# Kernel tuning notes

Measured on AMD Instinct MI355X. Metric: run time of the kernel, lower is better.

The kernel has to match this reference:

```python
import jax, jax.numpy as jnp
import numpy as np

B, T, IN, H, G, O, D = 64, 256, 256, 1024, 256, 64, 4
GO = G + O  # graph_size + out_channels = 320


def _lstm_cell(x, h, c, Wih, Whh, bih, bhh):
    # torch.nn.LSTMCell gate order: i, f, g, o
    g = x @ Wih.T + h @ Whh.T + (bih + bhh)
    i, f, gg, o = jnp.split(g, 4, axis=-1)
    c_new = jax.nn.sigmoid(f) * c + jax.nn.sigmoid(i) * jnp.tanh(gg)
    h_new = jax.nn.sigmoid(o) * jnp.tanh(c_new)
    return h_new, c_new


def _mlp(x, W1, b1, W2, b2, W3, b3):
    # make_mlp with linear_depth=3: Linear->SiLU->Linear->SiLU->Linear
    x = jax.nn.silu(x @ W1.T + b1)
    x = jax.nn.silu(x @ W2.T + b2)
    return x @ W3.T + b3


def setup_inputs() -> dict:
    key = jax.random.key(0)
    ks = iter(jax.random.split(key, 64))
    def p(shape, s=0.05):
        return jax.random.normal(next(ks), shape, jnp.float32) * s
    inp = {}
    inp["z"] = jax.random.normal(next(ks), (B, IN), jnp.float32)
    inp["m_true"] = jax.random.normal(next(ks), (B, T, GO), jnp.float32)
    for pre, od in (("eh", H), ("ec", H), ("ex", O)):
        inp[pre + "_W1"] = p((H, IN)); inp[pre + "_b1"] = p((H,))
        inp[pre + "_W2"] = p((H, H));  inp[pre + "_b2"] = p((H,))
        inp[pre + "_W3"] = p((od, H)); inp[pre + "_b3"] = p((od,))
    inp["in_Wih"] = p((4 * H, GO)); inp["in_Whh"] = p((4 * H, H))
    inp["in_bih"] = p((4 * H,));    inp["in_bhh"] = p((4 * H,))
    inp["rnns_Wih"] = p((D, 4 * H, H)); inp["rnns_Whh"] = p((D, 4 * H, H))
    inp["rnns_bih"] = p((D, 4 * H));    inp["rnns_bhh"] = p((D, 4 * H))
    inp["hA_W"] = p((D, H, H)); inp["hA_b"] = p((D, H))
    inp["cA_W"] = p((D, H, H)); inp["cA_b"] = p((D, H))
    inp["lastH_W"] = p((GO, H)); inp["lastH_b"] = p((GO,))
    inp["lastC_W"] = p((GO, H)); inp["lastC_b"] = p((GO,))
    inp["out_Wih"] = p((4 * GO, H)); inp["out_Whh"] = p((4 * GO, GO))
    inp["out_bih"] = p((4 * GO,));   inp["out_bhh"] = p((4 * GO,))
    return inp


def reference(z, m_true,
              eh_W1, eh_b1, eh_W2, eh_b2, eh_W3, eh_b3,
              ec_W1, ec_b1, ec_W2, ec_b2, ec_W3, ec_b3,
              ex_W1, ex_b1, ex_W2, ex_b2, ex_W3, ex_b3,
              in_Wih, in_Whh, in_bih, in_bhh,
              rnns_Wih, rnns_Whh, rnns_bih, rnns_bhh,
              hA_W, hA_b, cA_W, cA_b,
              lastH_W, lastH_b, lastC_W, lastC_b,
              out_Wih, out_Whh, out_bih, out_bhh):
    h0 = _mlp(z, eh_W1, eh_b1, eh_W2, eh_b2, eh_W3, eh_b3)
    c0 = _mlp(z, ec_W1, ec_b1, ec_W2, ec_b2, ec_W3, ec_b3)
    x_last = _mlp(z, ex_W1, ex_b1, ex_W2, ex_b2, ex_W3, ex_b3)
    m_hat0 = jnp.concatenate(
        [jnp.zeros((z.shape[0], G), z.dtype), x_last], axis=-1)  # [B, GO]
    # flip time, use first T-1 steps; time-major for scan: [T-1, B, GO]
    mt = jnp.flip(m_true, axis=1)[:, :-1, :].transpose(1, 0, 2)

    def step(carry, m_t):
        h0_, c0_ = carry
        h2, c2 = _lstm_cell(m_t, h0_, c0_, in_Wih, in_Whh, in_bih, in_bhh)
        c1 = c2
        for i in range(D):  # recurrent_depth inner chain (fixed, structural)
            h1 = h2 @ hA_W[i].T + hA_b[i]
            c1 = c2 @ cA_W[i].T + cA_b[i]
            h2, c2 = _lstm_cell(h2, h1, c1,
                                rnns_Wih[i], rnns_Whh[i],
                                rnns_bih[i], rnns_bhh[i])
        # note: original reuses c1 (last adapter output) for last_c_adapter
        hh = h2 @ lastH_W.T + lastH_b
        cc = c1 @ lastC_W.T + lastC_b
        ho, _ = _lstm_cell(h2, hh, cc, out_Wih, out_Whh, out_bih, out_bhh)
        return (h2, c2), ho

    _, outs = jax.lax.scan(step, (h0, c0), mt)  # outs: [T-1, B, GO]
    m_hat = jnp.concatenate([m_hat0[:, None, :], outs.transpose(1, 0, 2)],
                            axis=1)  # [B, T, GO]
    return m_hat
```

## Files before the change

### kernel.cpp

```cpp
#include <hip/hip_runtime.h>


typedef unsigned int u32;
typedef unsigned long long u64;
typedef unsigned short u16;
typedef __attribute__((ext_vector_type(8))) __bf16 bf16x8;
typedef __attribute__((ext_vector_type(4))) float f32x4;

#define DEVI __device__ __forceinline__

union FRAG { bf16x8 v; u16 s[8]; u64 q[2]; };
union P4 { u64 q; u16 s[4]; };
union F4 { u64 q[2]; float f[4]; };

DEVI u16 f2bf(float x){ u32 u = __float_as_uint(x); return (u16)((u + 0x7fffu + ((u>>16)&1u)) >> 16); }
DEVI float sigm(float x){ return 1.0f/(1.0f + __expf(-x)); }
DEVI float tanh_(float x){ return 2.0f/(1.0f + __expf(-2.0f*x)) - 1.0f; }
DEVI void ast(void* p, u64 v){ __hip_atomic_store((u64*)p, v, __ATOMIC_RELAXED, __HIP_MEMORY_SCOPE_AGENT); }

DEVI void ld16sc(FRAG& d, const void* p){
  asm volatile("global_load_dwordx4 %0, %1, off sc0 sc1" : "=v"(d.v) : "v"(p));
}
DEVI void ld16(FRAG& d, const void* p){
  asm volatile("global_load_dwordx4 %0, %1, off" : "=v"(d.v) : "v"(p));
}
DEVI void ldf4(f32x4& d, const void* p){
  asm volatile("global_load_dwordx4 %0, %1, off" : "=v"(d) : "v"(p));
}

#define MFMA16(a,b,c) __builtin_amdgcn_mfma_f32_16x16x32_bf16(a, b, c, 0, 0, 0)

#define NWG 168

#define SCHEDB() __builtin_amdgcn_sched_barrier(0)
#define WAITV(n) do{ SCHEDB(); \
  asm volatile("s_waitcnt vmcnt(" #n ")" ::: "memory"); \
  SCHEDB(); }while(0)

__global__ __launch_bounds__(256, 1) void k_scan(
    const float* __restrict__ m_true,
    const u16* __restrict__ Wcell, const u16* __restrict__ Win_h,
    const u16* __restrict__ Win_x, const u16* __restrict__ Wout,
    const u16* __restrict__ WccA,
    const float* __restrict__ b_in, const float* __restrict__ b_cell,
    const float* __restrict__ cAb, const float* __restrict__ b_out,
    const float* __restrict__ b_cc,
    u16* hS, u16* cS, float* cF, float* outp, u32* bar)
{
  const int wg = blockIdx.x;
  const int tid = threadIdx.x;
  const int wave = tid >> 6, lane = tid & 63;

  int pipe, lw;
  if (wg < 160){ pipe = (wg >> 3) & 1; lw = ((wg >> 4) << 3) | (wg & 7); }
  else         { pipe = (wg - 160) >> 2; lw = 80 + ((wg - 160) & 3); }

  const int bl = lane & 15, kg = lane >> 4;
  const int pair = wave >> 1;
  const int bt = (pipe << 1) + (wave & 1);
  const int b  = (bt << 4) + bl;
  const int swz = (bl & 7) << 4;
  const int foff = ((bl << 2) + kg) << 4;
  const int woff = (bt << 15) + ((lw >> 1) << 10) + (bl << 6) + ((lw & 1) << 5) + (kg << 3);
  u32* flagp = bar + (pipe*128 + lw)*32;
  const u32* fbase = bar + pipe*128*32;
  const int i2 = (lane < 20) ? 64 + lane : lane;
  __shared__ __align__(16) u16 ldsW[81920];

  f32x4 cprev = {0,0,0,0};
  f32x4 ccreg = {0,0,0,0};

  auto stage1 = [&](const u16* src, u16* lb, int segs){
    const u16* g = src + (lane << 3);
    u16* l = lb;
    for (int s = 0; s < segs; ++s){
      __builtin_amdgcn_global_load_lds(
          (const __attribute__((address_space(1))) void*)g,
          (__attribute__((address_space(3))) void*)l, 16, 0, 0);
      g += 512; l += 512;
    }
    SCHEDB();
  };
  auto afL = [&](const u16* lb, int row, int kb) -> bf16x8 {
    return *(const bf16x8*)((const char*)lb + row*512 + (kb ^ swz));
  };

  auto gsync = [&](u32 ep, const u16* pfsrc, int cstride, int spw, const u16* xsrc){
    SCHEDB();
    __syncthreads();
    if (tid == 0)
      __hip_atomic_store(flagp, ep, __ATOMIC_RELAXED, __HIP_MEMORY_SCOPE_AGENT);
    SCHEDB();
    if (pfsrc) stage1(pfsrc + (size_t)wave*cstride, ldsW + wave*cstride, spw);
    if (xsrc)  stage1(xsrc + wave*4096, ldsW + 65536 + wave*4096, 8);
    SCHEDB();
    if (wave == 0){
      for(;;){
        u32 a = __hip_atomic_load(fbase + lane*32, __ATOMIC_RELAXED, __HIP_MEMORY_SCOPE_AGENT);
        u32 c2 = __hip_atomic_load(fbase + i2*32, __ATOMIC_RELAXED, __HIP_MEMORY_SCOPE_AGENT);
        if (__all(a >= ep && c2 >= ep)) break;
        __builtin_amdgcn_s_sleep(1);
      }
    }
    __syncthreads();
    SCHEDB();
  };

  auto phase_incell = [&](int t, const u16* hIn, u16* hOut, u16* cOut){
    f32x4 A0={0,0,0,0}, A1={0,0,0,0}, A2={0,0,0,0}, A3={0,0,0,0};
    const char* hf = (const char*)hIn + (bt << 15) + foff;
    const int ksb = pair << 4;
    int jl = (kg << 2), jj = (lw << 4) + jl;
    FRAG sh[2][8], pa[8];
    f32x4 bg0, bg1, bg2, bg3;
    #pragma unroll
    for (int ks = 0; ks < 8; ++ks) ld16sc(sh[0][ks], hf + (ksb + ks)*1024);
    #pragma unroll
    for (int ks = 0; ks < 8; ++ks) ld16sc(sh[1][ks], hf + (ksb + 8 + ks)*1024);
    {
      const char* p2 = (const char*)(Win_x + (size_t)lw*20480 + 16384);
      #pragma unroll
      for (int k2 = 0; k2 < 2; ++k2)
        #pragma unroll
        for (int rb = 0; rb < 4; ++rb)
          ld16(pa[k2*4+rb], p2 + (rb*16 + bl)*128 + (((k2<<6)+(kg<<4)) ^ swz));
    }
    ldf4(bg0, b_in +        jj);
    ldf4(bg1, b_in + 1024 + jj);
    ldf4(bg2, b_in + 2048 + jj);
    ldf4(bg3, b_in + 3072 + jj);
    WAITV(20);
    const u16* lbA = ldsW + (pair*2)*16384;
    #pragma unroll
    for (int ks = 0; ks < 8; ++ks){
      int kb = (ks << 6) + (kg << 4);
      FRAG a;
      a.v = afL(lbA, bl, kb);      A0 = MFMA16(a.v, sh[0][ks].v, A0);
      a.v = afL(lbA, 16 + bl, kb); A1 = MFMA16(a.v, sh[0][ks].v, A1);
      a.v = afL(lbA, 32 + bl, kb); A2 = MFMA16(a.v, sh[0][ks].v, A2);
      a.v = afL(lbA, 48 + bl, kb); A3 = MFMA16(a.v, sh[0][ks].v, A3);
    }
    WAITV(12);
    const u16* lbB = ldsW + (pair*2+1)*16384;
    #pragma unroll
    for (int ks = 0; ks < 8; ++ks){
      int kb = (ks << 6) + (kg << 4);
      FRAG a;
      a.v = afL(lbB, bl, kb);      A0 = MFMA16(a.v, sh[1][ks].v, A0);
      a.v = afL(lbB, 16 + bl, kb); A1 = MFMA16(a.v, sh[1][ks].v, A1);
      a.v = afL(lbB, 32 + bl, kb); A2 = MFMA16(a.v, sh[1][ks].v, A2);
      a.v = afL(lbB, 48 + bl, kb); A3 = MFMA16(a.v, sh[1][ks].v, A3);
    }
    WAITV(4);
    if (wave >= 2){
      FRAG xf[10];
      const float* xr = m_true + (size_t)b*81920 + (size_t)(255 - t)*320;
      #pragma unroll
      for (int ks = 0; ks < 10; ++ks){
        int k = (ks << 5) + (kg << 3);
        f32x4 x0 = *(const f32x4*)(xr + k);
        f32x4 x1 = *(const f32x4*)(xr + k + 4);
        xf[ks].s[0]=f2bf(x0[0]); xf[ks].s[1]=f2bf(x0[1]); xf[ks].s[2]=f2bf(x0[2]); xf[ks].s[3]=f2bf(x0[3]);
        xf[ks].s[4]=f2bf(x1[0]); xf[ks].s[5]=f2bf(x1[1]); xf[ks].s[6]=f2bf(x1[2]); xf[ks].s[7]=f2bf(x1[3]);
      }
      const u16* lb4 = ldsW + 65536;
      #pragma unroll
      for (int ks = 0; ks < 8; ++ks){
        int kb = (ks << 6) + (kg << 4);
        FRAG a;
        a.v = afL(lb4, bl, kb);      A0 = MFMA16(a.v, xf[ks].v, A0);
        a.v = afL(lb4, 16 + bl, kb); A1 = MFMA16(a.v, xf[ks].v, A1);
        a.v = afL(lb4, 32 + bl, kb); A2 = MFMA16(a.v, xf[ks].v, A2);
        a.v = afL(lb4, 48 + bl, kb); A3 = MFMA16(a.v, xf[ks].v, A3);
      }
      #pragma unroll
      for (int k2 = 0; k2 < 2; ++k2){
        A0 = MFMA16(pa[k2*4+0].v, xf[8+k2].v, A0);
        A1 = MFMA16(pa[k2*4+1].v, xf[8+k2].v, A1);
        A2 = MFMA16(pa[k2*4+2].v, xf[8+k2].v, A2);
        A3 = MFMA16(pa[k2*4+3].v, xf[8+k2].v, A3);
      }
    }
    __syncthreads();
    float* red = (float*)ldsW;
    if (wave >= 2){
      float* r = red + ((wave&1)*64 + lane)*20;
      *(f32x4*)(r+0) = A0; *(f32x4*)(r+4) = A1;
      *(f32x4*)(r+8) = A2; *(f32x4*)(r+12) = A3;
    }
    __syncthreads();
    if (wave < 2){
      const float* r = red + ((wave&1)*64 + lane)*20;
      A0 += *(const f32x4*)(r+0); A1 += *(const f32x4*)(r+4);
      A2 += *(const f32x4*)(r+8); A3 += *(const f32x4*)(r+12);
      P4 hw, cw;
      #pragma unroll
      for (int rr = 0; rr < 4; ++rr){
        float gi = A0[rr] + bg0[rr];
        float gf = A1[rr] + bg1[rr];
        float gg = A2[rr] + bg2[rr];
        float go = A3[rr] + bg3[rr];
        float cn = sigm(gf)*cprev[rr] + sigm(gi)*tanh_(gg);
        hw.s[rr] = f2bf(sigm(go)*tanh_(cn));
        cw.s[rr] = f2bf(cn);
      }
      ast((char*)hOut + woff, hw.q);
      ast((char*)cOut + woff, cw.q);
    }
  };

  auto phase_cell = [&](int i, const u16* hIn, const u16* cIn, u16* hOut, u16* cOut, bool last){
    f32x4 A0={0,0,0,0}, A1={0,0,0,0}, A2={0,0,0,0}, A3={0,0,0,0}, A4={0,0,0,0};
    const char* hf  = (const char*)hIn + (bt << 15) + foff;
    const char* cfr = (const char*)cIn + (bt << 15) + foff;
    const int ksb = pair << 4;
    int jl = (kg << 2), jj = (lw << 4) + jl;
    FRAG sh[2][8], sc[2][8];
    f32x4 bg0, bg1, bg2, bg3, bca;
    #pragma unroll
    for (int ks = 0; ks < 8; ++ks) ld16sc(sh[0][ks], hf  + (ksb + ks)*1024);
    #pragma unroll
    for (int ks = 0; ks < 8; ++ks) ld16sc(sc[0][ks], cfr + (ksb + ks)*1024);
    #pragma unroll
    for (int ks = 0; ks < 8; ++ks) ld16sc(sh[1][ks], hf  + (ksb + 8 + ks)*1024);
    #pragma unroll
    for (int ks = 0; ks < 8; ++ks) ld16sc(sc[1][ks], cfr + (ksb + 8 + ks)*1024);
    ldf4(bg0, b_cell + i*4096 +        jj);
    ldf4(bg1, b_cell + i*4096 + 1024 + jj);
    ldf4(bg2, b_cell + i*4096 + 2048 + jj);
    ldf4(bg3, b_cell + i*4096 + 3072 + jj);
    ldf4(bca, cAb + i*1024 + jj);
    WAITV(21);
    const u16* lbA = ldsW + (pair*2)*20480;
    #pragma unroll
    for (int ks = 0; ks < 8; ++ks){
      int kb = (ks << 6) + (kg << 4);
      FRAG a;
      a.v = afL(lbA, bl, kb);      A0 = MFMA16(a.v, sh[0][ks].v, A0);
      a.v = afL(lbA, 16 + bl, kb); A1 = MFMA16(a.v, sh[0][ks].v, A1);
      a.v = afL(lbA, 32 + bl, kb); A2 = MFMA16(a.v, sh[0][ks].v, A2);
      a.v = afL(lbA, 48 + bl, kb); A3 = MFMA16(a.v, sh[0][ks].v, A3);
      a.v = afL(lbA, 64 + bl, kb); A4 = MFMA16(a.v, sc[0][ks].v, A4);
    }
    WAITV(5);
    const u16* lbB = ldsW + (pair*2+1)*20480;
    #pragma unroll
    for (int ks = 0; ks < 8; ++ks){
      int kb = (ks << 6) + (kg << 4);
      FRAG a;
      a.v = afL(lbB, bl, kb);      A0 = MFMA16(a.v, sh[1][ks].v, A0);
      a.v = afL(lbB, 16 + bl, kb); A1 = MFMA16(a.v, sh[1][ks].v, A1);
      a.v = afL(lbB, 32 + bl, kb); A2 = MFMA16(a.v, sh[1][ks].v, A2);
      a.v = afL(lbB, 48 + bl, kb); A3 = MFMA16(a.v, sh[1][ks].v, A3);
      a.v = afL(lbB, 64 + bl, kb); A4 = MFMA16(a.v, sc[1][ks].v, A4);
    }
    __syncthreads();
    float* red = (float*)ldsW;
    if (wave >= 2){
      float* r = red + ((wave&1)*64 + lane)*20;
      *(f32x4*)(r+0) = A0; *(f32x4*)(r+4) = A1;
      *(f32x4*)(r+8) = A2; *(f32x4*)(r+12) = A3; *(f32x4*)(r+16) = A4;
    }
    __syncthreads();
    if (wave < 2){
      const float* r = red + ((wave&1)*64 + lane)*20;
      A0 += *(const f32x4*)(r+0); A1 += *(const f32x4*)(r+4);
      A2 += *(const f32x4*)(r+8); A3 += *(const f32x4*)(r+12);
      A4 += *(const f32x4*)(r+16);
      P4 hw, cw; F4 cf4;
      #pragma unroll
      for (int rr = 0; rr < 4; ++rr){
        float gi = A0[rr] + bg0[rr];
        float gf = A1[rr] + bg1[rr];
        float gg = A2[rr] + bg2[rr];
        float go = A3[rr] + bg3[rr];
        float c1 = A4[rr] + bca[rr];
        float cn = sigm(gf)*c1 + sigm(gi)*tanh_(gg);
        hw.s[rr] = f2bf(sigm(go)*tanh_(cn));
        cw.s[rr] = f2bf(cn);
        cf4.f[rr] = cn;
      }
      ast((char*)hOut + woff, hw.q);
      ast((char*)cOut + woff, cw.q);
      if (last){ cprev[0]=cf4.f[0]; cprev[1]=cf4.f[1]; cprev[2]=cf4.f[2]; cprev[3]=cf4.f[3]; }
    }
  };

  auto phase_ccA = [&](const u16* cIn){
    f32x4 A = {0,0,0,0};
    const char* cfr = (const char*)cIn + (bt << 15) + foff;
    const int ksb = pair << 4;
    int jl = (kg << 2), jjo = ((lw - 64) << 4) + jl;
    FRAG sc[2][8];
    f32x4 bcc;
    #pragma unroll
    for (int ks = 0; ks < 8; ++ks) ld16sc(sc[0][ks], cfr + (ksb + ks)*1024);
    #pragma unroll
    for (int ks = 0; ks < 8; ++ks) ld16sc(sc[1][ks], cfr + (ksb + 8 + ks)*1024);
    ldf4(bcc, b_cc + jjo);
    WAITV(9);
    const u16* lbA = ldsW + (pair*2)*4096;
    #pragma unroll
    for (int ks = 0; ks < 8; ++ks){
      int kb = (ks << 6) + (kg << 4);
      FRAG a; a.v = afL(lbA, bl, kb);
      A = MFMA16(a.v, sc[0][ks].v, A);
    }
    WAITV(1);
    const u16* lbB = ldsW + (pair*2+1)*4096;
    #pragma unroll
    for (int ks = 0; ks < 8; ++ks){
      int kb = (ks << 6) + (kg << 4);
      FRAG a; a.v = afL(lbB, bl, kb);
      A = MFMA16(a.v, sc[1][ks].v, A);
    }
    __syncthreads();
    float* red = (float*)ldsW;
    if (wave >= 2) *(f32x4*)(red + ((wave&1)*64 + lane)*20) = A;
    __syncthreads();
    if (wave < 2){
      A += *(const f32x4*)(red + ((wave&1)*64 + lane)*20);
      #pragma unroll
      for (int rr = 0; rr < 4; ++rr) ccreg[rr] = A[rr] + bcc[rr];
    }
  };

  auto phase_out = [&](int t, const u16* hIn){
    f32x4 A0={0,0,0,0}, A1={0,0,0,0}, A2={0,0,0,0}, A3={0,0,0,0};
    const char* hf = (const char*)hIn + (bt << 15) + foff;
    const int ksb = pair << 4;
    int jl = (kg << 2), jjo = ((lw - 64) << 4) + jl;
    FRAG sh[2][8];
    f32x4 bg0, bg1, bg2, bg3;
    #pragma unroll
    for (int ks = 0; ks < 8; ++ks) ld16sc(sh[0][ks], hf + (ksb + ks)*1024);
    #pragma unroll
    for (int ks = 0; ks < 8; ++ks) ld16sc(sh[1][ks], hf + (ksb + 8 + ks)*1024);
    ldf4(bg0, b_out +       jjo);
    ldf4(bg1, b_out + 320 + jjo);
    ldf4(bg2, b_out + 640 + jjo);
    ldf4(bg3, b_out + 960 + jjo);
    WAITV(12);
    const u16* lbA = ldsW + (pair*2)*16384;
    #pragma unroll
    for (int ks = 0; ks < 8; ++ks){
      int kb = (ks << 6) + (kg << 4);
      FRAG a;
      a.v = afL(lbA, bl, kb);      A0 = MFMA16(a.v, sh[0][ks].v, A0);
      a.v = afL(lbA, 16 + bl, kb); A1 = MFMA16(a.v, sh[0][ks].v, A1);
      a.v = afL(lbA, 32 + bl, kb); A2 = MFMA16(a.v, sh[0][ks].v, A2);
      a.v = afL(lbA, 48 + bl, kb); A3 = MFMA16(a.v, sh[0][ks].v, A3);
    }
    WAITV(4);
    const u16* lbB = ldsW + (pair*2+1)*16384;
    #pragma unroll
    for (int ks = 0; ks < 8; ++ks){
      int kb = (ks << 6) + (kg << 4);
      FRAG a;
      a.v = afL(lbB, bl, kb);      A0 = MFMA16(a.v, sh[1][ks].v, A0);
      a.v = afL(lbB, 16 + bl, kb); A1 = MFMA16(a.v, sh[1][ks].v, A1);
      a.v = afL(lbB, 32 + bl, kb); A2 = MFMA16(a.v, sh[1][ks].v, A2);
      a.v = afL(lbB, 48 + bl, kb); A3 = MFMA16(a.v, sh[1][ks].v, A3);
    }
    __syncthreads();
    float* red = (float*)ldsW;
    if (wave >= 2){
      float* r = red + ((wave&1)*64 + lane)*20;
      *(f32x4*)(r+0) = A0; *(f32x4*)(r+4) = A1;
      *(f32x4*)(r+8) = A2; *(f32x4*)(r+12) = A3;
    }
    __syncthreads();
    if (wave < 2){
      const float* r = red + ((wave&1)*64 + lane)*20;
      A0 += *(const f32x4*)(r+0); A1 += *(const f32x4*)(r+4);
      A2 += *(const f32x4*)(r+8); A3 += *(const f32x4*)(r+12);
      f32x4 ho;
      #pragma unroll
      for (int rr = 0; rr < 4; ++rr){
        float gi = A0[rr] + bg0[rr];
        float gf = A1[rr] + bg1[rr];
        float gg = A2[rr] + bg2[rr];
        float go = A3[rr] + bg3[rr];
        float cn = sigm(gf)*ccreg[rr] + sigm(gi)*tanh_(gg);
        ho[rr] = sigm(go)*tanh_(cn);
      }
      *(f32x4*)(outp + (size_t)b*81920 + (size_t)(t+1)*320 + jjo) = ho;
    }
  };

  if (lw < 64){
    if (wave < 2){
      int jj = (lw << 4) + (kg << 2);
      cprev = *(const f32x4*)(cF + (size_t)b*1024 + jj);
    }
    stage1(Win_h + ((size_t)lw << 16) + wave*16384, ldsW + wave*16384, 32);
    stage1(Win_x + (size_t)lw*20480 + wave*4096, ldsW + 65536 + wave*4096, 8);
  }
  __syncthreads();
  SCHEDB();

  u16* hB0 = hS;        u16* hB1 = hS + 65536;
  u16* cB0 = cS;        u16* cB1 = cS + 65536;

  u32 ep = 1;
  if (lw < 64) phase_incell(0, hB1, hB0, cB0);
  gsync(ep++, (lw < 64) ? Wcell + (size_t)lw*81920 : nullptr, 20480, 40, nullptr);
  int p = 1;
  #pragma unroll 1
  for (int t = 0; t < 255; ++t){
    #pragma unroll 1
    for (int i = 0; i < 4; ++i){
      u16* hIn = (p & 1) ? hB0 : hB1;  u16* cIn = (p & 1) ? cB0 : cB1;
      u16* hOut = (p & 1) ? hB1 : hB0; u16* cOut = (p & 1) ? cB1 : cB0;
      if (lw < 64)      phase_cell(i, hIn, cIn, hOut, cOut, i == 3);
      else if (i == 3)  phase_ccA(cIn);
      const u16* pf = nullptr; const u16* xs = nullptr; int cstride = 0, spw = 0;
      if (lw < 64){
        if (i < 3){ pf = Wcell + (size_t)((i+1)*64 + lw)*81920; cstride = 20480; spw = 40; }
        else      { pf = Win_h + ((size_t)lw << 16); cstride = 16384; spw = 32;
                    xs = Win_x + (size_t)lw*20480; }
      } else {
        if (i == 2){ pf = WccA + ((size_t)(lw-64) << 14); cstride = 4096; spw = 8; }
        else if (i == 3){ pf = Wout + ((size_t)(lw-64) << 16); cstride = 16384; spw = 32; }
      }
      gsync(ep++, pf, cstride, spw, xs);
      ++p;
    }
    u16* hIn = (p & 1) ? hB0 : hB1;
    u16* hOut = (p & 1) ? hB1 : hB0; u16* cOut = (p & 1) ? cB1 : cB0;
    if (lw >= 64)       phase_out(t, hIn);
    else if (t < 254)   phase_incell(t + 1, hIn, hOut, cOut);
    gsync(ep++, (lw < 64 && t < 254) ? Wcell + (size_t)lw*81920 : nullptr, 20480, 40, nullptr);
    ++p;
  }
}


__global__ __launch_bounds__(256) void k_dense(const float* __restrict__ X, int xmode,
    const float* __restrict__ W, const float* __restrict__ bias,
    int OD, int ID, int act, int omode, float* outF, u16* outB)
{
  int o = blockIdx.x*4 + (threadIdx.x >> 6);
  if (o >= OD) return;
  int lane = threadIdx.x & 63;
  const float* wr = W + (size_t)o*ID;
  float acc = 0.f;
  if (xmode == 0){ for (int k = 0; k < ID; ++k) acc = fmaf(wr[k], X[(size_t)lane*ID + k], acc); }
  else           { for (int k = 0; k < ID; ++k) acc = fmaf(wr[k], X[(size_t)k*64 + lane], acc); }
  acc += bias[o];
  if (act) acc = acc * sigm(acc);
  if (omode == 0)      outF[(size_t)o*64 + lane] = acc;
  else if (omode == 1){
    int bt = lane >> 4, blx = lane & 15;
    outB[(size_t)bt*16384 + (size_t)(o>>5)*512 + blx*32 + ((o&31)>>3)*8 + (o&7)] = f2bf(acc);
  }
  else if (omode == 2) outF[(size_t)lane*1024 + o] = acc;
  else                 outF[(size_t)lane*81920 + 256 + o] = acc;
}

__global__ void k_zero0(float* out){ out[(size_t)blockIdx.x*81920 + threadIdx.x] = 0.f; }

__global__ __launch_bounds__(256) void k_tr(const float* __restrict__ in, u16* __restrict__ out, int M, int N){
  __shared__ u16 t[64][65];
  int m0 = blockIdx.x << 6, n0 = blockIdx.y << 6;
  int c = threadIdx.x & 63, rq = threadIdx.x >> 6;
  for (int rr = 0; rr < 16; ++rr){
    int r = (rq << 4) + rr;
    t[r][c] = f2bf(in[(size_t)(m0 + r)*N + n0 + c]);
  }
  __syncthreads();
  for (int rr = 0; rr < 16; ++rr){
    int r = (rq << 4) + rr;
    out[(size_t)(n0 + r)*M + m0 + c] = t[c][r];
  }
}

__global__ __launch_bounds__(256) void k_fuse(const float* __restrict__ Whh, const float* __restrict__ Wih,
    const u16* __restrict__ BT, int KM, int mode, u16* __restrict__ dst)
{
  int bx = blockIdx.x, by = blockIdx.y, bz = blockIdx.z;
  int lane = threadIdx.x & 63, wv = threadIdx.x >> 6;
  int bl = lane & 15, kg = lane >> 4;
  int jbase = (mode == 0) ? bz*1024 : ((mode == 1) ? bz*320 : 0);
  int jrow = jbase + bx*16 + bl;
  int k2c = by*64 + wv*16 + bl;
  f32x4 acc = {0,0,0,0};
  for (int m0 = 0; m0 < KM; m0 += 32){
    f32x4 wa0 = *(const f32x4*)(Whh + (size_t)jrow*KM + m0 + (kg << 3));
    f32x4 wa1 = *(const f32x4*)(Whh + (size_t)jrow*KM + m0 + (kg << 3) + 4);
    FRAG a;
    a.s[0]=f2bf(wa0[0]); a.s[1]=f2bf(wa0[1]); a.s[2]=f2bf(wa0[2]); a.s[3]=f2bf(wa0[3]);
    a.s[4]=f2bf(wa1[0]); a.s[5]=f2bf(wa1[1]); a.s[6]=f2bf(wa1[2]); a.s[7]=f2bf(wa1[3]);
    FRAG bb; bb.v = *(const bf16x8*)(BT + (size_t)k2c*KM + m0 + (kg << 3));
    acc = MFMA16(a.v, bb.v, acc);
  }
  #pragma unroll
  for (int r = 0; r < 4; ++r){
    int jl = (kg << 2) + r;
    int jg = jbase + bx*16 + jl;
    float v = acc[r];
    if (mode < 2) v += Wih[(size_t)jg*1024 + k2c];
    int re = (mode == 2) ? jl : (bz*16 + jl);
    int c = k2c >> 8, kl = k2c & 255;
    size_t pos;
    if (mode == 0)      pos = (size_t)bx*81920 + c*20480 + re*256 + (kl ^ ((re&7)<<3));
    else if (mode == 1) pos = (size_t)bx*65536 + c*16384 + re*256 + (kl ^ ((re&7)<<3));
    else                pos = (size_t)bx*16384 + c*4096  + re*256 + (kl ^ ((re&7)<<3));
    dst[pos] = f2bf(v);
  }
}

__global__ void k_pack_winh(const float* __restrict__ src, u16* __restrict__ dst){
  int id = blockIdx.x*256 + threadIdx.x;
  int j = id >> 10, k = id & 1023;
  int g = j >> 10, jj = j & 1023;
  int w = jj >> 4, r = (g << 4) + (jj & 15);
  int c = k >> 8, kl = k & 255;
  dst[(size_t)w*65536 + c*16384 + r*256 + (kl ^ ((r&7)<<3))] = f2bf(src[id]);
}

__global__ void k_pack_winx(const float* __restrict__ src, u16* __restrict__ dst){
  int j = blockIdx.x, k = threadIdx.x;
  int g = j >> 10, jj = j & 1023;
  int w = jj >> 4, r = (g << 4) + (jj & 15);
  float v = src[(size_t)j*320 + k];
  size_t pos;
  if (k < 256) pos = (size_t)w*20480 + r*256 + (k ^ ((r&7)<<3));
  else         pos = (size_t)w*20480 + 16384 + r*64 + ((k - 256) ^ ((r&7)<<3));
  dst[pos] = f2bf(v);
}

__global__ void k_pack_ca(const float* __restrict__ src, u16* __restrict__ dst){
  int id = blockIdx.x*256 + threadIdx.x;
  int jj = id >> 10, k = id & 1023;
  int w = jj >> 4, r = 64 + (jj & 15);
  int c = k >> 8, kl = k & 255;
  dst[(size_t)w*81920 + c*20480 + r*256 + (kl ^ ((r&7)<<3))] = f2bf(src[id]);
}

__global__ __launch_bounds__(256) void k_bias(const float* __restrict__ A, const float* __restrict__ x,
    const float* __restrict__ a1, const float* __restrict__ a2, float* __restrict__ o, int NJ, int K)
{
  int j = blockIdx.x*4 + (threadIdx.x >> 6);
  if (j >= NJ) return;
  int lane = threadIdx.x & 63;
  float acc = 0.f;
  if (A) for (int k = lane; k < K; k += 64) acc += A[(size_t)j*K + k]*x[k];
  for (int off = 32; off; off >>= 1) acc += __shfl_down(acc, off);
  if (lane == 0) o[j] = acc + (a1 ? a1[j] : 0.f) + (a2 ? a2[j] : 0.f);
}

extern "C" void kernel_launch(void* const* d_in, const int* in_sizes, int n_in,
                              void* d_out, int out_size, void* d_ws, size_t ws_size,
                              hipStream_t stream)
{
  (void)in_sizes; (void)n_in; (void)out_size;
  const float* z      = (const float*)d_in[0];
  const float* m_true = (const float*)d_in[1];
  const float* eh_W1=(const float*)d_in[2],  *eh_b1=(const float*)d_in[3];
  const float* eh_W2=(const float*)d_in[4],  *eh_b2=(const float*)d_in[5];
  const float* eh_W3=(const float*)d_in[6],  *eh_b3=(const float*)d_in[7];
  const float* ec_W1=(const float*)d_in[8],  *ec_b1=(const float*)d_in[9];
  const float* ec_W2=(const float*)d_in[10], *ec_b2=(const float*)d_in[11];
  const float* ec_W3=(const float*)d_in[12], *ec_b3=(const float*)d_in[13];
  const float* ex_W1=(const float*)d_in[14], *ex_b1=(const float*)d_in[15];
  const float* ex_W2=(const float*)d_in[16], *ex_b2=(const float*)d_in[17];
  const float* ex_W3=(const float*)d_in[18], *ex_b3=(const float*)d_in[19];
  const float* in_Wih=(const float*)d_in[20], *in_Whh=(const float*)d_in[21];
  const float* in_bih=(const float*)d_in[22], *in_bhh=(const float*)d_in[23];
  const float* r_Wih=(const float*)d_in[24],  *r_Whh=(const float*)d_in[25];
  const float* r_bih=(const float*)d_in[26],  *r_bhh=(const float*)d_in[27];
  const float* hA_W=(const float*)d_in[28],   *hA_b=(const float*)d_in[29];
  const float* cA_W=(const float*)d_in[30],   *cA_b=(const float*)d_in[31];
  const float* lastH_W=(const float*)d_in[32], *lastH_b=(const float*)d_in[33];
  const float* lastC_W=(const float*)d_in[34], *lastC_b=(const float*)d_in[35];
  const float* out_Wih=(const float*)d_in[36], *out_Whh=(const float*)d_in[37];
  const float* out_bih=(const float*)d_in[38], *out_bhh=(const float*)d_in[39];
  float* out = (float*)d_out;

  char* wsb = (char*)d_ws;
  size_t off = 0;
  auto alloc = [&](size_t bytes)->char*{
    char* p = wsb + off; off = (off + bytes + 255) & ~(size_t)255; return p;
  };
  u32* bar    = (u32*)alloc(256*32*4);
  u16* hS     = (u16*)alloc(2*64*1024*2);
  u16* cS     = (u16*)alloc(2*64*1024*2);
  float* cF   = (float*)alloc(64*1024*4);
  float* b_in = (float*)alloc(4096*4);
  float* b_cell=(float*)alloc(4*4096*4);
  float* b_out= (float*)alloc(1280*4);
  float* b_cc = (float*)alloc(320*4);
  float* t1   = (float*)alloc(1024*64*4);
  float* t2   = (float*)alloc(1024*64*4);
  u16* Tbuf   = (u16*)alloc((size_t)1024*1024*2);
  u16* Win_h  = (u16*)alloc((size_t)64*65536*2);
  u16* Win_x  = (u16*)alloc((size_t)64*20480*2);
  u16* Wcell  = (u16*)alloc((size_t)4*64*81920*2);
  u16* Wout   = (u16*)alloc((size_t)20*65536*2);
  u16* WccA   = (u16*)alloc((size_t)20*16384*2);
  if (off > ws_size) return;

  hipMemsetAsync(bar, 0, 256*32*4, stream);

  k_dense<<<256,256,0,stream>>>(z, 0, eh_W1, eh_b1, 1024, 256, 1, 0, t1, nullptr);
  k_dense<<<256,256,0,stream>>>(t1,1, eh_W2, eh_b2, 1024,1024, 1, 0, t2, nullptr);
  k_dense<<<256,256,0,stream>>>(t2,1, eh_W3, eh_b3, 1024,1024, 0, 1, nullptr, hS + 65536);
  k_dense<<<256,256,0,stream>>>(z, 0, ec_W1, ec_b1, 1024, 256, 1, 0, t1, nullptr);
  k_dense<<<256,256,0,stream>>>(t1,1, ec_W2, ec_b2, 1024,1024, 1, 0, t2, nullptr);
  k_dense<<<256,256,0,stream>>>(t2,1, ec_W3, ec_b3, 1024,1024, 0, 2, cF, nullptr);
  k_dense<<<256,256,0,stream>>>(z, 0, ex_W1, ex_b1, 1024, 256, 1, 0, t1, nullptr);
  k_dense<<<256,256,0,stream>>>(t1,1, ex_W2, ex_b2, 1024,1024, 1, 0, t2, nullptr);
  k_dense<<<16 ,256,0,stream>>>(t2,1, ex_W3, ex_b3,   64,1024, 0, 3, out, nullptr);
  k_zero0<<<64,256,0,stream>>>(out);

  k_pack_winh<<<16384,256,0,stream>>>(in_Whh, Win_h);
  k_pack_winx<<<4096,320,0,stream>>>(in_Wih, Win_x);
  for (int i = 0; i < 4; ++i)
    k_pack_ca<<<4096,256,0,stream>>>(cA_W + (size_t)i*1024*1024, Wcell + (size_t)i*64*81920);

  for (int i = 0; i < 4; ++i){
    k_tr<<<dim3(16,16),256,0,stream>>>(hA_W + (size_t)i*1024*1024, Tbuf, 1024, 1024);
    k_fuse<<<dim3(64,16,4),256,0,stream>>>(r_Whh + (size_t)i*4096*1024,
                                           r_Wih + (size_t)i*4096*1024,
                                           Tbuf, 1024, 0, Wcell + (size_t)i*64*81920);
  }
  k_tr<<<dim3(5,16),256,0,stream>>>(lastH_W, Tbuf, 320, 1024);
  k_fuse<<<dim3(20,16,4),256,0,stream>>>(out_Whh, out_Wih, Tbuf, 320, 1, Wout);
  k_tr<<<dim3(16,16),256,0,stream>>>(cA_W + (size_t)3*1024*1024, Tbuf, 1024, 1024);
  k_fuse<<<dim3(20,16,1),256,0,stream>>>(lastC_W, nullptr, Tbuf, 1024, 2, WccA);

  k_bias<<<1024,256,0,stream>>>(nullptr, nullptr, in_bih, in_bhh, b_in, 4096, 0);
  for (int i = 0; i < 4; ++i)
    k_bias<<<1024,256,0,stream>>>(r_Whh + (size_t)i*4096*1024, hA_b + i*1024,
                                  r_bih + i*4096, r_bhh + i*4096, b_cell + i*4096, 4096, 1024);
  k_bias<<<320,256,0,stream>>>(out_Whh, lastH_b, out_bih, out_bhh, b_out, 1280, 320);
  k_bias<<<80 ,256,0,stream>>>(lastC_W, cA_b + 3*1024, lastC_b, nullptr, b_cc, 320, 1024);

  k_scan<<<NWG,256,0,stream>>>(m_true, Wcell, Win_h, Win_x, Wout, WccA,
                               b_in, b_cell, cA_b, b_out, b_cc,
                               hS, cS, cF, out, bar);
}
```

Measured before the change: 11.81 ms.

## Split grid barrier into per-wave flags and overlap weight staging with signaling

Replaces the block-wide grid-sync lambda with macros. Waves 0 and 1 each publish their own flag as soon as their own global stores have retired (tracked by a vmcnt wait), instead of waiting on a full __syncthreads first. The next phase's weight staging into LDS is now issued before or alongside the flag store. The flag array doubles to two slots per workgroup, so the poll loop reads three flags per lane. A workgroup barrier is added right before each phase's first LDS read so the staged weights are visible. The goal is to shorten the critical path of the 1000+ grid-wide barriers in the recurrent scan, at the cost of more flag traffic and more subtle memory-ordering assumptions.

Measured after the change: 15.31 ms. 1.3x slower.

```diff
diff --git a/kernel.cpp b/kernel.cpp
--- a/kernel.cpp
+++ b/kernel.cpp
@@ -36,6 +36,37 @@
 #define WAITV(n) do{ SCHEDB(); \
   asm volatile("s_waitcnt vmcnt(" #n ")" ::: "memory"); \
   SCHEDB(); }while(0)
+#define RBAR() do{ SCHEDB(); __builtin_amdgcn_s_barrier(); SCHEDB(); }while(0)
+
+#define POLL(epv) \
+  if (wave == 0){ \
+    for(;;){ \
+      u32 a0 = __hip_atomic_load(fbase + lane*32,      __ATOMIC_RELAXED, __HIP_MEMORY_SCOPE_AGENT); \
+      u32 a1 = __hip_atomic_load(fbase + (lane+64)*32, __ATOMIC_RELAXED, __HIP_MEMORY_SCOPE_AGENT); \
+      u32 a2 = __hip_atomic_load(fbase + i2x*32,       __ATOMIC_RELAXED, __HIP_MEMORY_SCOPE_AGENT); \
+      if (__all(a0 >= (epv) && a1 >= (epv) && a2 >= (epv))) break; \
+      __builtin_amdgcn_s_sleep(1); \
+    } \
+  }
+
+#define GSYNC_CELL(epv, SLIT, STAGE_STMT) do{ \
+  RBAR(); \
+  STAGE_STMT; SCHEDB(); \
+  if (wave < 2){ WAITV(SLIT); \
+    if (lane == 0) __hip_atomic_store(flagp + wave*32, (epv), __ATOMIC_RELAXED, __HIP_MEMORY_SCOPE_AGENT); } \
+  SCHEDB(); \
+  POLL(epv); \
+  RBAR(); \
+}while(0)
+
+#define GSYNC_OUT(epv, STAGE_STMT) do{ \
+  RBAR(); \
+  if (wave < 2 && lane == 0) \
+    __hip_atomic_store(flagp + wave*32, (epv), __ATOMIC_RELAXED, __HIP_MEMORY_SCOPE_AGENT); \
+  STAGE_STMT; SCHEDB(); \
+  POLL(epv); \
+  RBAR(); \
+}while(0)
 
 __global__ __launch_bounds__(256, 1) void k_scan(
     const float* __restrict__ m_true,
@@ -62,9 +93,9 @@
   const int swz = (bl & 7) << 4;
   const int foff = ((bl << 2) + kg) << 4;
   const int woff = (bt << 15) + ((lw >> 1) << 10) + (bl << 6) + ((lw & 1) << 5) + (kg << 3);
-  u32* flagp = bar + (pipe*128 + lw)*32;
-  const u32* fbase = bar + pipe*128*32;
-  const int i2 = (lane < 20) ? 64 + lane : lane;
+  u32* flagp = bar + (pipe*176 + lw*2)*32;
+  const u32* fbase = bar + pipe*176*32;
+  const int i2x = (lane < 40) ? lane + 128 : lane;
   __shared__ __align__(16) u16 ldsW[81920];
 
   f32x4 cprev = {0,0,0,0};
@@ -85,27 +116,6 @@
     return *(const bf16x8*)((const char*)lb + row*512 + (kb ^ swz));
   };
 
-  auto gsync = [&](u32 ep, const u16* pfsrc, int cstride, int spw, const u16* xsrc){
-    SCHEDB();
-    __syncthreads();
-    if (tid == 0)
-      __hip_atomic_store(flagp, ep, __ATOMIC_RELAXED, __HIP_MEMORY_SCOPE_AGENT);
-    SCHEDB();
-    if (pfsrc) stage1(pfsrc + (size_t)wave*cstride, ldsW + wave*cstride, spw);
-    if (xsrc)  stage1(xsrc + wave*4096, ldsW + 65536 + wave*4096, 8);
-    SCHEDB();
-    if (wave == 0){
-      for(;;){
-        u32 a = __hip_atomic_load(fbase + lane*32, __ATOMIC_RELAXED, __HIP_MEMORY_SCOPE_AGENT);
-        u32 c2 = __hip_atomic_load(fbase + i2*32, __ATOMIC_RELAXED, __HIP_MEMORY_SCOPE_AGENT);
-        if (__all(a >= ep && c2 >= ep)) break;
-        __builtin_amdgcn_s_sleep(1);
-      }
-    }
-    __syncthreads();
-    SCHEDB();
-  };
-
   auto phase_incell = [&](int t, const u16* hIn, u16* hOut, u16* cOut){
     f32x4 A0={0,0,0,0}, A1={0,0,0,0}, A2={0,0,0,0}, A3={0,0,0,0};
     const char* hf = (const char*)hIn + (bt << 15) + foff;
@@ -130,6 +140,7 @@
     ldf4(bg2, b_in + 2048 + jj);
     ldf4(bg3, b_in + 3072 + jj);
     WAITV(20);
+    RBAR();
     const u16* lbA = ldsW + (pair*2)*16384;
     #pragma unroll
     for (int ks = 0; ks < 8; ++ks){
@@ -231,6 +242,7 @@
     ldf4(bg3, b_cell + i*4096 + 3072 + jj);
     ldf4(bca, cAb + i*1024 + jj);
     WAITV(21);
+    RBAR();
     const u16* lbA = ldsW + (pair*2)*20480;
     #pragma unroll
     for (int ks = 0; ks < 8; ++ks){
@@ -299,6 +311,7 @@
     for (int ks = 0; ks < 8; ++ks) ld16sc(sc[1][ks], cfr + (ksb + 8 + ks)*1024);
     ldf4(bcc, b_cc + jjo);
     WAITV(9);
+    RBAR();
     const u16* lbA = ldsW + (pair*2)*4096;
     #pragma unroll
     for (int ks = 0; ks < 8; ++ks){
@@ -341,6 +354,7 @@
     ldf4(bg2, b_out + 640 + jjo);
     ldf4(bg3, b_out + 960 + jjo);
     WAITV(12);
+    RBAR();
     const u16* lbA = ldsW + (pair*2)*16384;
     #pragma unroll
     for (int ks = 0; ks < 8; ++ks){
@@ -403,8 +417,13 @@
   u16* cB0 = cS;        u16* cB1 = cS + 65536;
 
   u32 ep = 1;
-  if (lw < 64) phase_incell(0, hB1, hB0, cB0);
-  gsync(ep++, (lw < 64) ? Wcell + (size_t)lw*81920 : nullptr, 20480, 40, nullptr);
+  if (lw < 64){
+    phase_incell(0, hB1, hB0, cB0);
+    GSYNC_CELL(ep, 40, stage1(Wcell + (size_t)lw*81920 + (size_t)wave*20480, ldsW + wave*20480, 40));
+  } else {
+    GSYNC_OUT(ep, (void)0);
+  }
+  ++ep;
   int p = 1;
   #pragma unroll 1
   for (int t = 0; t < 255; ++t){
@@ -412,26 +431,42 @@
     for (int i = 0; i < 4; ++i){
       u16* hIn = (p & 1) ? hB0 : hB1;  u16* cIn = (p & 1) ? cB0 : cB1;
       u16* hOut = (p & 1) ? hB1 : hB0; u16* cOut = (p & 1) ? cB1 : cB0;
-      if (lw < 64)      phase_cell(i, hIn, cIn, hOut, cOut, i == 3);
-      else if (i == 3)  phase_ccA(cIn);
-      const u16* pf = nullptr; const u16* xs = nullptr; int cstride = 0, spw = 0;
       if (lw < 64){
-        if (i < 3){ pf = Wcell + (size_t)((i+1)*64 + lw)*81920; cstride = 20480; spw = 40; }
-        else      { pf = Win_h + ((size_t)lw << 16); cstride = 16384; spw = 32;
-                    xs = Win_x + (size_t)lw*20480; }
+        phase_cell(i, hIn, cIn, hOut, cOut, i == 3);
+        if (i < 3){
+          GSYNC_CELL(ep, 40, stage1(Wcell + (size_t)((i+1)*64 + lw)*81920 + (size_t)wave*20480, ldsW + wave*20480, 40));
+        } else {
+          GSYNC_CELL(ep, 40, {
+            stage1(Win_h + ((size_t)lw << 16) + wave*16384, ldsW + wave*16384, 32);
+            stage1(Win_x + (size_t)lw*20480 + wave*4096, ldsW + 65536 + wave*4096, 8);
+          });
+        }
       } else {
-        if (i == 2){ pf = WccA + ((size_t)(lw-64) << 14); cstride = 4096; spw = 8; }
-        else if (i == 3){ pf = Wout + ((size_t)(lw-64) << 16); cstride = 16384; spw = 32; }
-      }
-      gsync(ep++, pf, cstride, spw, xs);
-      ++p;
+        if (i == 3) phase_ccA(cIn);
+        if (i == 2){
+          GSYNC_OUT(ep, stage1(WccA + ((size_t)(lw-64) << 14) + wave*4096, ldsW + wave*4096, 8));
+        } else if (i == 3){
+          GSYNC_OUT(ep, stage1(Wout + ((size_t)(lw-64) << 16) + wave*16384, ldsW + wave*16384, 32));
+        } else {
+          GSYNC_OUT(ep, (void)0);
+        }
+      }
+      ++ep; ++p;
     }
     u16* hIn = (p & 1) ? hB0 : hB1;
     u16* hOut = (p & 1) ? hB1 : hB0; u16* cOut = (p & 1) ? cB1 : cB0;
-    if (lw >= 64)       phase_out(t, hIn);
-    else if (t < 254)   phase_incell(t + 1, hIn, hOut, cOut);
-    gsync(ep++, (lw < 64 && t < 254) ? Wcell + (size_t)lw*81920 : nullptr, 20480, 40, nullptr);
-    ++p;
+    if (lw >= 64){
+      phase_out(t, hIn);
+      GSYNC_OUT(ep, (void)0);
+    } else {
+      if (t < 254){
+        phase_incell(t + 1, hIn, hOut, cOut);
+        GSYNC_CELL(ep, 40, stage1(Wcell + (size_t)lw*81920 + (size_t)wave*20480, ldsW + wave*20480, 40));
+      } else {
+        GSYNC_CELL(ep, 0, (void)0);
+      }
+    }
+    ++ep; ++p;
   }
 }
 
@@ -583,7 +618,7 @@
   auto alloc = [&](size_t bytes)->char*{
     char* p = wsb + off; off = (off + bytes + 255) & ~(size_t)255; return p;
   };
-  u32* bar    = (u32*)alloc(256*32*4);
+  u32* bar    = (u32*)alloc(512*32*4);
   u16* hS     = (u16*)alloc(2*64*1024*2);
   u16* cS     = (u16*)alloc(2*64*1024*2);
   float* cF   = (float*)alloc(64*1024*4);
@@ -601,7 +636,7 @@
   u16* WccA   = (u16*)alloc((size_t)20*16384*2);
   if (off > ws_size) return;
 
-  hipMemsetAsync(bar, 0, 256*32*4, stream);
+  hipMemsetAsync(bar, 0, 512*32*4, stream);
 
   k_dense<<<256,256,0,stream>>>(z, 0, eh_W1, eh_b1, 1024, 256, 1, 0, t1, nullptr);
   k_dense<<<256,256,0,stream>>>(t1,1, eh_W2, eh_b2, 1024,1024, 1, 0, t2, nullptr);
```
